# Optimization experiments

Hardware: AMD Instinct MI355X
Metric: run time of the kernel (lower is better)

## Reference

```python
import jax, jax.numpy as jnp
import numpy as np

BN_INV = 1.0 / np.sqrt(1.0 + 1e-5)  # eval-mode BatchNorm1d with running_mean=0, running_var=1


def _lin_bn_relu(x, W, g, b):
    # Linear(no bias) -> BN(eval) -> ReLU
    return jax.nn.relu((x @ W.T) * (g * BN_INV) + b)


def setup_inputs() -> dict:
    key = jax.random.key(0)
    ks = jax.random.split(key, 24)
    B, P, N, C, H, OUT = 8, 1024, 20, 32, 256, 256
    s = 0.05
    inp = {
        "polylines": jax.random.normal(ks[0], (B, P, N, C), dtype=jnp.float32),
        "polylines_mask": jax.random.randint(ks[1], (B, P, N), 0, 2) > 0,
        # pre_mlps: [Lin(C->H,no bias)+BN+ReLU] x2, Lin(H->H, bias)
        "pre_w0": jax.random.normal(ks[2], (H, C), dtype=jnp.float32) * s,
        "pre_g0": jnp.ones((H,), jnp.float32),
        "pre_b0": jnp.zeros((H,), jnp.float32),
        "pre_w1": jax.random.normal(ks[3], (H, H), dtype=jnp.float32) * s,
        "pre_g1": jnp.ones((H,), jnp.float32),
        "pre_b1": jnp.zeros((H,), jnp.float32),
        "pre_w2": jax.random.normal(ks[4], (H, H), dtype=jnp.float32) * s,
        "pre_bias2": jnp.zeros((H,), jnp.float32),
        # mlps: c_in=2H -> [H,H,H]
        "mlp_w0": jax.random.normal(ks[5], (H, 2 * H), dtype=jnp.float32) * s,
        "mlp_g0": jnp.ones((H,), jnp.float32),
        "mlp_b0": jnp.zeros((H,), jnp.float32),
        "mlp_w1": jax.random.normal(ks[6], (H, H), dtype=jnp.float32) * s,
        "mlp_g1": jnp.ones((H,), jnp.float32),
        "mlp_b1": jnp.zeros((H,), jnp.float32),
        "mlp_w2": jax.random.normal(ks[7], (H, H), dtype=jnp.float32) * s,
        "mlp_bias2": jnp.zeros((H,), jnp.float32),
        # out_mlps (without_norm): Lin(H->H,bias)+ReLU, Lin(H->OUT,bias)
        "out_w0": jax.random.normal(ks[8], (H, H), dtype=jnp.float32) * s,
        "out_b0": jnp.zeros((H,), jnp.float32),
        "out_w1": jax.random.normal(ks[9], (OUT, H), dtype=jnp.float32) * s,
        "out_b1": jnp.zeros((OUT,), jnp.float32),
    }
    return inp


def reference(polylines, polylines_mask,
              pre_w0, pre_g0, pre_b0, pre_w1, pre_g1, pre_b1, pre_w2, pre_bias2,
              mlp_w0, mlp_g0, mlp_b0, mlp_w1, mlp_g1, mlp_b1, mlp_w2, mlp_bias2,
              out_w0, out_b0, out_w1, out_b1):
    # gather->MLP->zero-scatter is equivalent to dense MLP followed by mask-zeroing
    # (all per-point ops are elementwise / last-dim matmuls).
    m = polylines_mask[..., None].astype(polylines.dtype)  # (B,P,N,1)

    x = _lin_bn_relu(polylines, pre_w0, pre_g0, pre_b0)
    x = _lin_bn_relu(x, pre_w1, pre_g1, pre_b1)
    x = (x @ pre_w2.T + pre_bias2) * m                      # (B,P,N,H) zero at invalid

    pooled = x.max(axis=2)                                  # (B,P,H) max over zero-filled buffer
    x = jnp.concatenate(
        [x, jnp.broadcast_to(pooled[:, :, None, :], x.shape)], axis=-1)  # (B,P,N,2H)

    x = _lin_bn_relu(x, mlp_w0, mlp_g0, mlp_b0)
    x = _lin_bn_relu(x, mlp_w1, mlp_g1, mlp_b1)
    x = (x @ mlp_w2.T + mlp_bias2) * m                      # (B,P,N,H)

    buf = x.max(axis=2)                                     # (B,P,H)

    valid = jnp.any(polylines_mask, axis=-1)                # sum(mask)>0
    y = jax.nn.relu(buf @ out_w0.T + out_b0)
    y = (y @ out_w1.T + out_b1) * valid[..., None].astype(buf.dtype)  # (B,P,OUT)
    return y
```

## Files before the change

kernel.cpp:

```cpp
#include <hip/hip_runtime.h>
#include <stdint.h>
#include <stddef.h>

typedef __bf16 bf16;
typedef __bf16 bf16x4 __attribute__((ext_vector_type(4)));
typedef __bf16 bf16x8 __attribute__((ext_vector_type(8)));
typedef float f32x4 __attribute__((ext_vector_type(4)));
typedef float f32x16 __attribute__((ext_vector_type(16)));

#define BNI 0.9999950000374996f
#define NROW 240
#define NPOLYB 12
#define TOTROW 163840
#define NPOLY 8192
#define NBLK 683

#define AADDR(r, ch) ((r)*256 + ((((ch) ^ ((r)&31)))<<3))

#define OFF_ACT  0
#define OFF_WB0  122880
#define OFF_WB1  139264
#define OFF_T2   155648
#define OFF_VAL  161792
#define LDS_TOTAL 161840

#define WS_PRE_W0 0
#define WS_PRE_W1 8192
#define WS_PRE_W2 73728
#define WS_MLP_W0 139264
#define WS_MLP_W1 270336
#define WS_MLP_W2 335872
#define WS_OUT_W0 401408
#define WS_OUT_W1 466944

__device__ __forceinline__ bf16 f2b(float f){
  unsigned int i = __builtin_bit_cast(unsigned int, f);
  unsigned int r = i + 0x7fffu + ((i >> 16) & 1u);
  unsigned short h = (unsigned short)(r >> 16);
  return __builtin_bit_cast(bf16, h);
}
__device__ __forceinline__ float b2f(bf16 x){
  unsigned short u = __builtin_bit_cast(unsigned short, x);
  union { unsigned int i; float f; } v; v.i = ((unsigned int)u) << 16; return v.f;
}
__device__ __forceinline__ bf16x8 ld8f(const float* p, float sc){
  f32x4 a = *(const f32x4*)p;
  f32x4 b = *(const f32x4*)(p + 4);
  bf16x8 r;
  #pragma unroll
  for (int j = 0; j < 4; ++j){ r[j] = f2b(a[j]*sc); r[4+j] = f2b(b[j]*sc); }
  return r;
}

__global__ __launch_bounds__(256)
void prep_kernel(const float* s0, const float* s1, const float* s2, const float* s3,
                 const float* s4, const float* s5, const float* s6, const float* s7,
                 const float* g0, const float* g1, const float* g3, const float* g4,
                 bf16* dst)
{
  const int offs[8] = {WS_PRE_W0, WS_PRE_W1, WS_PRE_W2, WS_MLP_W0,
                       WS_MLP_W1, WS_MLP_W2, WS_OUT_W0, WS_OUT_W1};
  const int sz[8]   = {8192, 65536, 65536, 131072, 65536, 65536, 65536, 65536};
  const int ld[8]   = {32, 256, 256, 512, 256, 256, 256, 256};
  int r = blockIdx.y;
  const float* src = s0;
  if (r == 1) src = s1; else if (r == 2) src = s2; else if (r == 3) src = s3;
  else if (r == 4) src = s4; else if (r == 5) src = s5; else if (r == 6) src = s6;
  else if (r == 7) src = s7;
  const float* gp = (r==0)?g0:(r==1)?g1:(r==3)?g3:(r==4)?g4:nullptr;
  int i = (blockIdx.x*256 + threadIdx.x)*8;
  if (i < sz[r]){
    float sc = gp ? gp[i/ld[r]]*BNI : 1.0f;
    *(bf16x8*)&dst[offs[r] + i] = ld8f(src + i, sc);
  }
}

__device__ __forceinline__ void stageAsync32(const bf16* W, int ldK, int nt, bf16* buf, int tid){
  int wv = tid >> 6;
  #pragma unroll
  for (int i = 0; i < 2; ++i){
    int id = tid + 512*i;
    int fr = id >> 5, kcd = id & 31;
    int kcs = kcd ^ (fr & 31);
    const bf16* g = W + (size_t)(nt*32 + fr)*ldK + kcs*8;
    bf16* l = buf + (size_t)(wv*64 + 512*i)*8;
    __builtin_amdgcn_global_load_lds(
        (const __attribute__((address_space(1))) void*)g,
        (__attribute__((address_space(3))) void*)l,
        16, 0, 0);
  }
}

template<int RELU, int MASK, int ADDT2>
__device__ __forceinline__ void epiT(
    const f32x16& acc, int nt, int row, int poly, float mk, bool valid,
    bf16* sAct, const bf16* sT2, const float* bptr, int hi)
{
  #pragma unroll
  for (int q2 = 0; q2 < 4; ++q2){
    int f0 = nt*32 + 8*q2 + 4*hi;
    f32x4 bb = *(const f32x4*)(bptr + f0);
    bf16x4 tv = {};
    if (ADDT2) tv = *(const bf16x4*)&sT2[poly*256 + f0];
    bf16x4 o;
    #pragma unroll
    for (int j = 0; j < 4; ++j){
      float v = acc[4*q2 + j];
      if (ADDT2) v += b2f(tv[j]);
      v += bb[j];
      if (RELU) v = fmaxf(v, 0.0f);
      if (MASK) v *= mk;
      o[j] = f2b(v);
    }
    if (valid)
      *(bf16x4*)&sAct[row*256 + (((nt*4 + q2) ^ (row & 31))<<3) + 4*hi] = o;
  }
}

template<int RELU, int MASK, int ADDT2>
__device__ __forceinline__ void layerT(
    bf16* sAct, bf16* wb0, bf16* wb1, const bf16* sT2,
    const bf16* W, int ldK, const float* bptr,
    const int* maskp, int blk, int row, int rowc, int lane32, int hi, int tid)
{
  bf16x8 B[16];
  #pragma unroll
  for (int t = 0; t < 16; ++t)
    B[t] = *(const bf16x8*)&sAct[AADDR(rowc, 2*t + hi)];

  float mk = 1.0f;
  if (MASK){
    int g = blk*NROW + row;
    mk = (row < NROW && g < TOTROW && maskp[g]) ? 1.0f : 0.0f;
  }
  const int poly = rowc/20;
  const bool valid = row < NROW;

  stageAsync32(W, ldK, 0, wb0, tid);
  __syncthreads();
  #pragma unroll 1
  for (int c = 0; c < 8; ++c){
    const bf16* cur = (c & 1) ? wb1 : wb0;
    bf16* nxt = (c & 1) ? wb0 : wb1;
    if (c < 7) stageAsync32(W, ldK, c + 1, nxt, tid);
    bf16x8 wf[16];
    const bf16* base = cur + lane32*256;
    #pragma unroll
    for (int t = 0; t < 16; ++t)
      wf[t] = *(const bf16x8*)(base + (((2*t + hi) ^ (lane32 & 31))<<3));
    f32x16 acc = {};
    #pragma unroll
    for (int t = 0; t < 16; ++t)
      acc = __builtin_amdgcn_mfma_f32_32x32x16_bf16(wf[t], B[t], acc, 0, 0, 0);
    epiT<RELU,MASK,ADDT2>(acc, c, row, poly, mk, valid, sAct, sT2, bptr, hi);
    __syncthreads();
  }
}

__device__ __forceinline__ void poolT(const bf16* sAct, bf16* sPool, int tid){
  if (tid < 384){
    int poly = tid >> 5, c = tid & 31;
    float m[8];
    bf16x8 v0 = *(const bf16x8*)&sAct[AADDR(poly*20, c)];
    #pragma unroll
    for (int j = 0; j < 8; ++j) m[j] = b2f(v0[j]);
    for (int r = 1; r < 20; ++r){
      bf16x8 v = *(const bf16x8*)&sAct[AADDR(poly*20 + r, c)];
      #pragma unroll
      for (int j = 0; j < 8; ++j) m[j] = fmaxf(m[j], b2f(v[j]));
    }
    bf16x8 o;
    #pragma unroll
    for (int j = 0; j < 8; ++j) o[j] = f2b(m[j]);
    *(bf16x8*)&sPool[AADDR(poly, c)] = o;
  }
}

__global__ __launch_bounds__(512) __attribute__((amdgpu_waves_per_eu(2, 2)))
void traj_kernel(const float* __restrict__ poly, const int* __restrict__ maskp,
                 const float* pre_b0, const float* pre_b1, const float* pre_bias2,
                 const float* mlp_b0, const float* mlp_b1, const float* mlp_bias2,
                 const float* out_b0, const float* out_b1,
                 const bf16* __restrict__ ws,
                 float* __restrict__ outp)
{
  extern __shared__ char smem[];
  bf16*  sAct   = (bf16*)(smem + OFF_ACT);
  bf16*  wb0    = (bf16*)(smem + OFF_WB0);
  bf16*  wb1    = (bf16*)(smem + OFF_WB1);
  bf16*  sT2    = (bf16*)(smem + OFF_T2);
  float* sValid = (float*)(smem + OFF_VAL);
  bf16*  sPool  = wb0;
  bf16*  sY     = sAct;

  const int tid = threadIdx.x;
  const int w = tid >> 6, L = tid & 63, lane32 = L & 31, hi = L >> 5;
  const int row  = w*32 + lane32;
  const int rowc = row < NROW ? row : NROW - 1;
  const int blk = blockIdx.x;

  const bf16* pw0 = ws + WS_PRE_W0;
  const bf16* pw1 = ws + WS_PRE_W1;
  const bf16* pw2 = ws + WS_PRE_W2;
  const bf16* mw0 = ws + WS_MLP_W0;
  const bf16* mw1 = ws + WS_MLP_W1;
  const bf16* mw2 = ws + WS_MLP_W2;
  const bf16* ow0 = ws + WS_OUT_W0;
  const bf16* ow1 = ws + WS_OUT_W1;

  #pragma unroll
  for (int i = 0; i < 2; ++i){
    int id = tid + 512*i;
    if (id < 960){
      int r = id >> 2, c = id & 3;
      int grow = blk*NROW + r;
      bf16x8 v = {};
      if (grow < TOTROW) v = ld8f(poly + (size_t)grow*32 + c*8, 1.0f);
      *(bf16x8*)&sAct[AADDR(r, c)] = v;
    }
  }
  __syncthreads();
  if (tid < NPOLYB){
    float v = 0.0f;
    #pragma unroll
    for (int r = 0; r < 20; ++r){
      int g = blk*NROW + tid*20 + r;
      if (g < TOTROW && maskp[g]) v = 1.0f;
    }
    sValid[tid] = v;
  }

  {
    bf16x8 B0 = *(const bf16x8*)&sAct[AADDR(rowc, hi)];
    bf16x8 B1 = *(const bf16x8*)&sAct[AADDR(rowc, 2 + hi)];
    #pragma unroll 1
    for (int nt = 0; nt < 8; ++nt){
      const bf16* p = pw0 + (size_t)(nt*32 + lane32)*32 + 8*hi;
      bf16x8 w0 = *(const bf16x8*)p;
      bf16x8 w1 = *(const bf16x8*)(p + 16);
      f32x16 acc = {};
      acc = __builtin_amdgcn_mfma_f32_32x32x16_bf16(w0, B0, acc, 0, 0, 0);
      acc = __builtin_amdgcn_mfma_f32_32x32x16_bf16(w1, B1, acc, 0, 0, 0);
      epiT<1,0,0>(acc, nt, row, 0, 1.0f, row < NROW, sAct, sT2, pre_b0, hi);
    }
  }
  __syncthreads();

  layerT<1,0,0>(sAct, wb0, wb1, sT2, pw1, 256, pre_b1,    maskp, blk, row, rowc, lane32, hi, tid);
  layerT<0,1,0>(sAct, wb0, wb1, sT2, pw2, 256, pre_bias2, maskp, blk, row, rowc, lane32, hi, tid);

  poolT(sAct, sPool, tid);
  __syncthreads();

  {
    bf16x8 Bp[16];
    #pragma unroll
    for (int t = 0; t < 16; ++t)
      Bp[t] = *(const bf16x8*)&sPool[AADDR((lane32 < NPOLYB ? lane32 : 0), 2*t + hi)];
    int nt = w;
    const bf16* p = mw0 + (size_t)(nt*32 + lane32)*512 + 256 + 8*hi;
    f32x16 acc = {};
    #pragma unroll
    for (int t = 0; t < 16; ++t){
      bf16x8 wf = *(const bf16x8*)(p + 16*t);
      acc = __builtin_amdgcn_mfma_f32_32x32x16_bf16(wf, Bp[t], acc, 0, 0, 0);
    }
    if (lane32 < NPOLYB){
      #pragma unroll
      for (int q2 = 0; q2 < 4; ++q2){
        int f0 = nt*32 + 8*q2 + 4*hi;
        bf16x4 o;
        #pragma unroll
        for (int j = 0; j < 4; ++j) o[j] = f2b(acc[4*q2 + j]);
        *(bf16x4*)&sT2[lane32*256 + f0] = o;
      }
    }
  }
  __syncthreads();

  layerT<1,0,1>(sAct, wb0, wb1, sT2, mw0, 512, mlp_b0,    maskp, blk, row, rowc, lane32, hi, tid);
  layerT<1,0,0>(sAct, wb0, wb1, sT2, mw1, 256, mlp_b1,    maskp, blk, row, rowc, lane32, hi, tid);
  layerT<0,1,0>(sAct, wb0, wb1, sT2, mw2, 256, mlp_bias2, maskp, blk, row, rowc, lane32, hi, tid);

  poolT(sAct, sPool, tid);
  __syncthreads();

  {
    bf16x8 Bp[16];
    #pragma unroll
    for (int t = 0; t < 16; ++t)
      Bp[t] = *(const bf16x8*)&sPool[AADDR((lane32 < NPOLYB ? lane32 : 0), 2*t + hi)];
    int nt = w;
    const bf16* p = ow0 + (size_t)(nt*32 + lane32)*256 + 8*hi;
    f32x16 acc = {};
    #pragma unroll
    for (int t = 0; t < 16; ++t){
      bf16x8 wf = *(const bf16x8*)(p + 16*t);
      acc = __builtin_amdgcn_mfma_f32_32x32x16_bf16(wf, Bp[t], acc, 0, 0, 0);
    }
    if (lane32 < NPOLYB){
      #pragma unroll
      for (int q2 = 0; q2 < 4; ++q2){
        int f0 = nt*32 + 8*q2 + 4*hi;
        f32x4 bb = *(const f32x4*)(out_b0 + f0);
        bf16x4 o;
        #pragma unroll
        for (int j = 0; j < 4; ++j) o[j] = f2b(fmaxf(acc[4*q2 + j] + bb[j], 0.0f));
        *(bf16x4*)&sY[lane32*256 + (((nt*4 + q2) ^ (lane32 & 31))<<3) + 4*hi] = o;
      }
    }
  }
  __syncthreads();

  {
    bf16x8 By[16];
    #pragma unroll
    for (int t = 0; t < 16; ++t)
      By[t] = *(const bf16x8*)&sY[AADDR((lane32 < NPOLYB ? lane32 : 0), 2*t + hi)];
    int gp = blk*NPOLYB + lane32;
    float vd = (lane32 < NPOLYB) ? sValid[lane32] : 0.0f;
    int nt = w;
    const bf16* p = ow1 + (size_t)(nt*32 + lane32)*256 + 8*hi;
    f32x16 acc = {};
    #pragma unroll
    for (int t = 0; t < 16; ++t){
      bf16x8 wf = *(const bf16x8*)(p + 16*t);
      acc = __builtin_amdgcn_mfma_f32_32x32x16_bf16(wf, By[t], acc, 0, 0, 0);
    }
    if (lane32 < NPOLYB && gp < NPOLY){
      #pragma unroll
      for (int q2 = 0; q2 < 4; ++q2){
        int f0 = nt*32 + 8*q2 + 4*hi;
        f32x4 bb = *(const f32x4*)(out_b1 + f0);
        f32x4 o;
        #pragma unroll
        for (int j = 0; j < 4; ++j) o[j] = (acc[4*q2 + j] + bb[j]) * vd;
        *(f32x4*)&outp[(size_t)gp*256 + f0] = o;
      }
    }
  }
}

extern "C" void kernel_launch(void* const* d_in, const int* in_sizes, int n_in,
                              void* d_out, int out_size, void* d_ws, size_t ws_size,
                              hipStream_t stream)
{
  const float* poly      = (const float*)d_in[0];
  const int*   maskp     = (const int*)  d_in[1];
  const float* pre_w0    = (const float*)d_in[2];
  const float* pre_g0    = (const float*)d_in[3];
  const float* pre_b0    = (const float*)d_in[4];
  const float* pre_w1    = (const float*)d_in[5];
  const float* pre_g1    = (const float*)d_in[6];
  const float* pre_b1    = (const float*)d_in[7];
  const float* pre_w2    = (const float*)d_in[8];
  const float* pre_bias2 = (const float*)d_in[9];
  const float* mlp_w0    = (const float*)d_in[10];
  const float* mlp_g0    = (const float*)d_in[11];
  const float* mlp_b0    = (const float*)d_in[12];
  const float* mlp_w1    = (const float*)d_in[13];
  const float* mlp_g1    = (const float*)d_in[14];
  const float* mlp_b1    = (const float*)d_in[15];
  const float* mlp_w2    = (const float*)d_in[16];
  const float* mlp_bias2 = (const float*)d_in[17];
  const float* out_w0    = (const float*)d_in[18];
  const float* out_b0    = (const float*)d_in[19];
  const float* out_w1    = (const float*)d_in[20];
  const float* out_b1    = (const float*)d_in[21];

  bf16* ws = (bf16*)d_ws;

  (void)hipFuncSetAttribute((const void*)&traj_kernel,
                            hipFuncAttributeMaxDynamicSharedMemorySize, LDS_TOTAL);

  prep_kernel<<<dim3(64, 8), dim3(256), 0, stream>>>(
      pre_w0, pre_w1, pre_w2, mlp_w0, mlp_w1, mlp_w2, out_w0, out_w1,
      pre_g0, pre_g1, mlp_g0, mlp_g1, ws);

  traj_kernel<<<dim3(NBLK), dim3(512), LDS_TOTAL, stream>>>(
      poly, maskp,
      pre_b0, pre_b1, pre_bias2,
      mlp_b0, mlp_b1, mlp_bias2,
      out_b0, out_b1,
      ws, (float*)d_out);
}
```

Before: 303.9 us.

## Split weight staging into K-half chunks with triple-buffered async pipeline

```diff
diff --git a/kernel.cpp b/kernel.cpp
--- a/kernel.cpp
+++ b/kernel.cpp
@@ -18,11 +18,10 @@
 #define AADDR(r, ch) ((r)*256 + ((((ch) ^ ((r)&31)))<<3))
 
 #define OFF_ACT  0
-#define OFF_WB0  122880
-#define OFF_WB1  139264
-#define OFF_T2   155648
-#define OFF_VAL  161792
-#define LDS_TOTAL 161840
+#define OFF_WB   122880
+#define OFF_T2   147456
+#define OFF_VAL  153600
+#define LDS_TOTAL 153648
 
 #define WS_PRE_W0 0
 #define WS_PRE_W1 8192
@@ -32,6 +31,11 @@
 #define WS_MLP_W2 335872
 #define WS_OUT_W0 401408
 #define WS_OUT_W1 466944
+
+#define PIPE_BAR(NSTR) do{ \
+    asm volatile("s_waitcnt lgkmcnt(0)\n\ts_waitcnt vmcnt(" NSTR ")" ::: "memory"); \
+    __builtin_amdgcn_s_barrier(); \
+    __builtin_amdgcn_sched_barrier(0); }while(0)
 
 __device__ __forceinline__ bf16 f2b(float f){
   unsigned int i = __builtin_bit_cast(unsigned int, f);
@@ -75,20 +79,17 @@
   }
 }
 
-__device__ __forceinline__ void stageAsync32(const bf16* W, int ldK, int nt, bf16* buf, int tid){
+__device__ __forceinline__ void stage8(const bf16* W, int ldK, int c, bf16* buf, int tid){
+  int nt = c >> 1, kh = c & 1;
+  int fr = tid >> 4, kc = tid & 15;
+  int kcs = kc ^ (fr & 15);
+  const bf16* g = W + (size_t)(nt*32 + fr)*ldK + kh*128 + kcs*8;
   int wv = tid >> 6;
-  #pragma unroll
-  for (int i = 0; i < 2; ++i){
-    int id = tid + 512*i;
-    int fr = id >> 5, kcd = id & 31;
-    int kcs = kcd ^ (fr & 31);
-    const bf16* g = W + (size_t)(nt*32 + fr)*ldK + kcs*8;
-    bf16* l = buf + (size_t)(wv*64 + 512*i)*8;
-    __builtin_amdgcn_global_load_lds(
-        (const __attribute__((address_space(1))) void*)g,
-        (__attribute__((address_space(3))) void*)l,
-        16, 0, 0);
-  }
+  bf16* l = buf + (size_t)(wv*64)*8;
+  __builtin_amdgcn_global_load_lds(
+      (const __attribute__((address_space(1))) void*)g,
+      (__attribute__((address_space(3))) void*)l,
+      16, 0, 0);
 }
 
 template<int RELU, int MASK, int ADDT2>
@@ -118,8 +119,8 @@
 }
 
 template<int RELU, int MASK, int ADDT2>
-__device__ __forceinline__ void layerT(
-    bf16* sAct, bf16* wb0, bf16* wb1, const bf16* sT2,
+__device__ __forceinline__ void layerP(
+    bf16* sAct, bf16* wb, const bf16* sT2,
     const bf16* W, int ldK, const float* bptr,
     const int* maskp, int blk, int row, int rowc, int lane32, int hi, int tid)
 {
@@ -136,24 +137,40 @@
   const int poly = rowc/20;
   const bool valid = row < NROW;
 
-  stageAsync32(W, ldK, 0, wb0, tid);
-  __syncthreads();
+  stage8(W, ldK, 0, wb,        tid);
+  stage8(W, ldK, 1, wb + 4096, tid);
+  PIPE_BAR("1");
   #pragma unroll 1
-  for (int c = 0; c < 8; ++c){
-    const bf16* cur = (c & 1) ? wb1 : wb0;
-    bf16* nxt = (c & 1) ? wb0 : wb1;
-    if (c < 7) stageAsync32(W, ldK, c + 1, nxt, tid);
-    bf16x8 wf[16];
-    const bf16* base = cur + lane32*256;
-    #pragma unroll
-    for (int t = 0; t < 16; ++t)
-      wf[t] = *(const bf16x8*)(base + (((2*t + hi) ^ (lane32 & 31))<<3));
-    f32x16 acc = {};
-    #pragma unroll
-    for (int t = 0; t < 16; ++t)
-      acc = __builtin_amdgcn_mfma_f32_32x32x16_bf16(wf[t], B[t], acc, 0, 0, 0);
-    epiT<RELU,MASK,ADDT2>(acc, c, row, poly, mk, valid, sAct, sT2, bptr, hi);
-    __syncthreads();
+  for (int p = 0; p < 8; ++p){
+    const int c0 = 2*p;
+    const bf16* cur0 = wb + (size_t)(c0 % 3)*4096;
+    const bf16* cur1 = wb + (size_t)((c0+1) % 3)*4096;
+    bf16* n0 = wb + (size_t)((c0+2) % 3)*4096;
+    bf16* n1 = wb + (size_t)((c0+3) % 3)*4096;
+    f32x16 acc;
+    if (p < 7) stage8(W, ldK, c0+2, n0, tid);
+    {
+      const bf16* base = cur0 + lane32*128;
+      #pragma unroll
+      for (int j = 0; j < 16; ++j) acc[j] = 0.0f;
+      #pragma unroll
+      for (int t = 0; t < 8; ++t){
+        bf16x8 wf = *(const bf16x8*)(base + (((2*t + hi) ^ (lane32 & 15))<<3));
+        acc = __builtin_amdgcn_mfma_f32_32x32x16_bf16(wf, B[t], acc, 0, 0, 0);
+      }
+    }
+    if (p < 7) PIPE_BAR("1"); else PIPE_BAR("0");
+    if (p < 7) stage8(W, ldK, c0+3, n1, tid);
+    {
+      const bf16* base = cur1 + lane32*128;
+      #pragma unroll
+      for (int t = 0; t < 8; ++t){
+        bf16x8 wf = *(const bf16x8*)(base + (((2*t + hi) ^ (lane32 & 15))<<3));
+        acc = __builtin_amdgcn_mfma_f32_32x32x16_bf16(wf, B[8 + t], acc, 0, 0, 0);
+      }
+      epiT<RELU,MASK,ADDT2>(acc, p, row, poly, mk, valid, sAct, sT2, bptr, hi);
+    }
+    if (p < 7) PIPE_BAR("1"); else PIPE_BAR("0");
   }
 }
 
@@ -186,11 +203,10 @@
 {
   extern __shared__ char smem[];
   bf16*  sAct   = (bf16*)(smem + OFF_ACT);
-  bf16*  wb0    = (bf16*)(smem + OFF_WB0);
-  bf16*  wb1    = (bf16*)(smem + OFF_WB1);
+  bf16*  wb     = (bf16*)(smem + OFF_WB);
   bf16*  sT2    = (bf16*)(smem + OFF_T2);
   float* sValid = (float*)(smem + OFF_VAL);
-  bf16*  sPool  = wb0;
+  bf16*  sPool  = wb;
   bf16*  sY     = sAct;
 
   const int tid = threadIdx.x;
@@ -246,8 +262,8 @@
   }
   __syncthreads();
 
-  layerT<1,0,0>(sAct, wb0, wb1, sT2, pw1, 256, pre_b1,    maskp, blk, row, rowc, lane32, hi, tid);
-  layerT<0,1,0>(sAct, wb0, wb1, sT2, pw2, 256, pre_bias2, maskp, blk, row, rowc, lane32, hi, tid);
+  layerP<1,0,0>(sAct, wb, sT2, pw1, 256, pre_b1,    maskp, blk, row, rowc, lane32, hi, tid);
+  layerP<0,1,0>(sAct, wb, sT2, pw2, 256, pre_bias2, maskp, blk, row, rowc, lane32, hi, tid);
 
   poolT(sAct, sPool, tid);
   __syncthreads();
@@ -278,9 +294,9 @@
   }
   __syncthreads();
 
-  layerT<1,0,1>(sAct, wb0, wb1, sT2, mw0, 512, mlp_b0,    maskp, blk, row, rowc, lane32, hi, tid);
-  layerT<1,0,0>(sAct, wb0, wb1, sT2, mw1, 256, mlp_b1,    maskp, blk, row, rowc, lane32, hi, tid);
-  layerT<0,1,0>(sAct, wb0, wb1, sT2, mw2, 256, mlp_bias2, maskp, blk, row, rowc, lane32, hi, tid);
+  layerP<1,0,1>(sAct, wb, sT2, mw0, 512, mlp_b0,    maskp, blk, row, rowc, lane32, hi, tid);
+  layerP<1,0,0>(sAct, wb, sT2, mw1, 256, mlp_b1,    maskp, blk, row, rowc, lane32, hi, tid);
+  layerP<0,1,0>(sAct, wb, sT2, mw2, 256, mlp_bias2, maskp, blk, row, rowc, lane32, hi, tid);
 
   poolT(sAct, sPool, tid);
   __syncthreads();
```

Result: slower. 327.7 us (+7.8%).
